# Kernel tuning notes

Hardware: AMD Instinct MI355X
Metric: run time of the kernel (lower is better)

## Reference

```python
import jax, jax.numpy as jnp
import numpy as np

GRID_H, GRID_W, BOX, CLASSES = 13, 13, 5, 80
COORD_FACTOR, NO_OBJECT_FACTOR, OBJECT_FACTOR, CLASS_FACTOR = 1.0, 1.0, 5.0, 1.0
ANCHORS = jnp.array([0.57273, 0.677385, 1.87446, 2.06253, 3.33843, 5.47434,
                     7.88282, 3.52778, 9.77052, 9.16828], dtype=jnp.float32)


def setup_inputs() -> dict:
    key = jax.random.key(0)
    k1, k2, k3 = jax.random.split(key, 3)
    B, T = 256, 50
    y_true = jax.random.uniform(k1, (B, GRID_H, GRID_W, BOX, 5 + CLASSES), dtype=jnp.float32)
    y_pred = jax.random.normal(k2, (B, GRID_H, GRID_W, BOX, 5 + CLASSES), dtype=jnp.float32)
    true_boxes = jax.random.uniform(k3, (B, 1, 1, 1, T, 4), dtype=jnp.float32)
    return {"y_true": y_true, "y_pred": y_pred, "true_boxes": true_boxes}


def reference(y_true, y_pred, true_boxes):
    f32 = jnp.float32
    anchors = ANCHORS.reshape(1, 1, 1, BOX, 2)
    # cell grid exactly as in torch: tile(range(13), 13).reshape(1,13,13,1,1)
    cell_w = jnp.tile(jnp.arange(GRID_H, dtype=f32), (GRID_W,)).reshape(1, GRID_H, GRID_W, 1, 1)
    cell_h = jnp.transpose(cell_w, (0, 2, 1, 3, 4))
    cell_grid = jnp.concatenate([cell_w, cell_h], axis=-1)  # [1,13,13,1,2]

    pred_box_xy = jax.nn.sigmoid(y_pred[..., :2]) + cell_grid          # [B,13,13,5,2]
    pred_box_wh = jnp.exp(y_pred[..., 2:4]) * anchors                  # [B,13,13,5,2]
    pred_box_conf = jax.nn.sigmoid(y_pred[..., 4])                      # [B,13,13,5]
    pred_box_class = y_pred[..., 5:]                                    # [B,13,13,5,80]

    true_box_xy = y_true[..., 0:2]
    true_box_wh = y_true[..., 2:4]

    # IoU between pred and matched true box per anchor cell
    t_half = true_box_wh / 2.0
    t_mins, t_maxes = true_box_xy - t_half, true_box_xy + t_half
    p_half = pred_box_wh / 2.0
    p_mins, p_maxes = pred_box_xy - p_half, pred_box_xy + p_half
    i_wh = jnp.maximum(jnp.minimum(p_maxes, t_maxes) - jnp.maximum(p_mins, t_mins), 0.0)
    i_areas = i_wh[..., 0] * i_wh[..., 1]
    union = pred_box_wh[..., 0] * pred_box_wh[..., 1] + true_box_wh[..., 0] * true_box_wh[..., 1] - i_areas
    iou = i_areas / union
    true_box_conf = iou * y_true[..., 4]
    true_box_class = jnp.argmax(y_true[..., 5:], axis=-1)               # [B,13,13,5]

    coord_mask = y_true[..., 4:5] * COORD_FACTOR                        # [B,13,13,5,1]

    # broadcast IoU vs all true boxes -> [B,13,13,5,T]
    tb_xy, tb_wh = true_boxes[..., 0:2], true_boxes[..., 2:4]
    tb_half = tb_wh / 2.0
    tb_mins, tb_maxes = tb_xy - tb_half, tb_xy + tb_half
    pxy = pred_box_xy[:, :, :, :, None, :]                               # [B,13,13,5,1,2]
    pwh = pred_box_wh[:, :, :, :, None, :]
    pw_half = pwh / 2.0
    pb_mins, pb_maxes = pxy - pw_half, pxy + pw_half
    bi_wh = jnp.maximum(jnp.minimum(pb_maxes, tb_maxes) - jnp.maximum(pb_mins, tb_mins), 0.0)
    bi_areas = bi_wh[..., 1] * bi_wh[..., 0]
    b_union = pwh[..., 0] * pwh[..., 1] + tb_wh[..., 0] * tb_wh[..., 1] - bi_areas
    best_ious = jnp.max(bi_areas / b_union, axis=4)                      # [B,13,13,5]

    conf_mask = (best_ious < 0.6).astype(f32) * (1.0 - y_true[..., 4]) * NO_OBJECT_FACTOR
    conf_mask = conf_mask + true_box_conf * OBJECT_FACTOR
    class_mask = y_true[..., 4] * CLASS_FACTOR

    nb_coord = jnp.sum((coord_mask > 0.0).astype(f32))
    nb_conf = jnp.sum((conf_mask > 0.0).astype(f32))
    nb_class = jnp.sum((class_mask > 0.0).astype(f32))

    loss_xy = jnp.sum(jnp.square(true_box_xy - pred_box_xy) * coord_mask) / (nb_coord + 1e-6) / 2.0
    loss_wh = jnp.sum(jnp.square(true_box_wh - pred_box_wh) * coord_mask) / (nb_coord + 1e-6) / 2.0
    loss_conf = jnp.sum(jnp.square(true_box_conf - pred_box_conf) * conf_mask) / (nb_conf + 1e-6) / 2.0

    logp = jax.nn.log_softmax(pred_box_class, axis=-1)                   # [B,13,13,5,80]
    ce = -jnp.take_along_axis(logp, true_box_class[..., None], axis=-1)[..., 0]
    loss_class = jnp.sum(ce * class_mask) / (nb_class + 1e-6)

    return loss_xy + loss_wh + loss_conf + loss_class
```

## Files before the change

kernel.cpp:

```cpp
#include <hip/hip_runtime.h>
#include <math.h>

#define GRID_HW   13
#define NBOX      5
#define NCLASS    80
#define REC       85
#define CPB_CELLS (GRID_HW*GRID_HW*NBOX)
#define T_BOXES   50
#define CPB       64
#define THREADS   256

__device__ __constant__ float c_anchors[10] = {
    0.57273f, 0.677385f, 1.87446f, 2.06253f, 3.33843f,
    5.47434f, 7.88282f, 3.52778f, 9.77052f, 9.16828f};

template <int USE_ATOMIC>
__global__ __launch_bounds__(THREADS)
void yolo_loss_main(const float* __restrict__ y_true,
                    const float* __restrict__ y_pred,
                    const float* __restrict__ tboxes,
                    double* __restrict__ partials,
                    int n_cells)
{
    __shared__ float lds_yt[CPB * REC];
    __shared__ float lds_yp[CPB * REC];
    __shared__ double red[4][7];

    const int tid   = threadIdx.x;
    const int cell0 = blockIdx.x * CPB;

    {
        const size_t base = (size_t)cell0 * REC;
        long long avail_ll = (long long)n_cells * REC - (long long)base;
        int navail = (avail_ll > (long long)(CPB * REC)) ? (CPB * REC)
                    : (avail_ll < 0 ? 0 : (int)avail_ll);
        int n4 = navail >> 2;
        const float4* gt = (const float4*)(y_true + base);
        const float4* gp = (const float4*)(y_pred + base);
        float4* st = (float4*)lds_yt;
        float4* sp = (float4*)lds_yp;
        for (int i = tid; i < n4; i += THREADS) { st[i] = gt[i]; sp[i] = gp[i]; }
        for (int i = (n4 << 2) + tid; i < navail; i += THREADS) {
            lds_yt[i] = y_true[base + i];
            lds_yp[i] = y_pred[base + i];
        }
    }
    __syncthreads();

    const int q    = tid & 3;
    const int quad = tid >> 2;
    const int cell = cell0 + quad;

    double p_xy = 0.0, p_wh = 0.0, p_conf = 0.0, p_ce = 0.0;
    double p_nc = 0.0, p_nf = 0.0, p_ncl = 0.0;

    if (cell < n_cells) {
        int b    = cell / CPB_CELLS;
        int rem  = cell - b * CPB_CELLS;
        int h    = rem / (GRID_HW * NBOX);
        int rem2 = rem - h * (GRID_HW * NBOX);
        int w    = rem2 / NBOX;
        int box  = rem2 - w * NBOX;

        const float* yt = lds_yt + quad * REC;
        const float* yp = lds_yp + quad * REC;

        const float yt4 = yt[4];
        const float tx = yt[0], ty = yt[1], tw = yt[2], th = yt[3];

        const float px = 1.f / (1.f + expf(-yp[0])) + (float)w;
        const float py = 1.f / (1.f + expf(-yp[1])) + (float)h;
        const float pw = expf(yp[2]) * c_anchors[2 * box];
        const float ph = expf(yp[3]) * c_anchors[2 * box + 1];
        const float pconf = 1.f / (1.f + expf(-yp[4]));

        const float pw2 = pw * 0.5f, ph2 = ph * 0.5f;
        const float p_minx = px - pw2, p_maxx = px + pw2;
        const float p_miny = py - ph2, p_maxy = py + ph2;

        float tw2 = tw * 0.5f, th2 = th * 0.5f;
        float iw = fmaxf(fminf(p_maxx, tx + tw2) - fmaxf(p_minx, tx - tw2), 0.f);
        float ih = fmaxf(fminf(p_maxy, ty + th2) - fmaxf(p_miny, ty - th2), 0.f);
        float inter = iw * ih;
        float iou = inter / (pw * ph + tw * th - inter);
        const float true_conf = iou * yt4;

        float amax = -INFINITY; int aidx = 0x7fffffff;
        #pragma unroll
        for (int k = 0; k < NCLASS / 4; ++k) {
            int c = q + 4 * k;
            float v = yt[5 + c];
            if (v > amax) { amax = v; aidx = c; }
        }
        #pragma unroll
        for (int m = 1; m <= 2; m <<= 1) {
            float ov = __shfl_xor(amax, m);
            int   oi = __shfl_xor(aidx, m);
            if (ov > amax || (ov == amax && oi < aidx)) { amax = ov; aidx = oi; }
        }

        float lmax = -INFINITY;
        #pragma unroll
        for (int k = 0; k < NCLASS / 4; ++k)
            lmax = fmaxf(lmax, yp[5 + q + 4 * k]);
        #pragma unroll
        for (int m = 1; m <= 2; m <<= 1)
            lmax = fmaxf(lmax, __shfl_xor(lmax, m));
        float lsum = 0.f;
        #pragma unroll
        for (int k = 0; k < NCLASS / 4; ++k)
            lsum += expf(yp[5 + q + 4 * k] - lmax);
        #pragma unroll
        for (int m = 1; m <= 2; m <<= 1)
            lsum += __shfl_xor(lsum, m);
        const float ce = -(yp[5 + aidx] - lmax - logf(lsum));

        const float4* tb = (const float4*)(tboxes + (size_t)b * T_BOXES * 4);
        float best = -INFINITY;
        for (int t = q; t < T_BOXES; t += 4) {
            float4 bx = tb[t];
            float bw2 = bx.z * 0.5f, bh2 = bx.w * 0.5f;
            float iw2 = fmaxf(fminf(p_maxx, bx.x + bw2) - fmaxf(p_minx, bx.x - bw2), 0.f);
            float ih2 = fmaxf(fminf(p_maxy, bx.y + bh2) - fmaxf(p_miny, bx.y - bh2), 0.f);
            float ia = iw2 * ih2;
            float r  = ia / (pw * ph + bx.z * bx.w - ia);
            best = fmaxf(best, r);
        }
        #pragma unroll
        for (int m = 1; m <= 2; m <<= 1)
            best = fmaxf(best, __shfl_xor(best, m));

        if (q == 0) {
            const float cm = yt4;
            p_xy = (double)(((tx - px) * (tx - px) + (ty - py) * (ty - py)) * cm);
            p_wh = (double)(((tw - pw) * (tw - pw) + (th - ph) * (th - ph)) * cm);
            float conf_mask = ((best < 0.6f) ? 1.f : 0.f) * (1.f - yt4)
                            + true_conf * 5.f;
            p_conf = (double)((true_conf - pconf) * (true_conf - pconf) * conf_mask);
            p_ce   = (double)(ce * yt4);
            p_nc   = (cm > 0.f)        ? 1.0 : 0.0;
            p_nf   = (conf_mask > 0.f) ? 1.0 : 0.0;
            p_ncl  = (yt4 > 0.f)       ? 1.0 : 0.0;
        }
    }

    double v[7] = {p_xy, p_wh, p_conf, p_ce, p_nc, p_nf, p_ncl};
    #pragma unroll
    for (int k = 0; k < 7; ++k) {
        #pragma unroll
        for (int off = 32; off > 0; off >>= 1)
            v[k] += __shfl_down(v[k], off);
    }
    const int wave = tid >> 6, lane = tid & 63;
    if (lane == 0) {
        #pragma unroll
        for (int k = 0; k < 7; ++k) red[wave][k] = v[k];
    }
    __syncthreads();
    if (tid < 7) {
        double s = red[0][tid] + red[1][tid] + red[2][tid] + red[3][tid];
        if (USE_ATOMIC) {
            unsafeAtomicAdd(&partials[tid], s);
        } else {
            partials[(size_t)blockIdx.x * 8 + tid] = s;
        }
    }
}

template <int USE_ATOMIC>
__global__ __launch_bounds__(256)
void yolo_loss_final(const double* __restrict__ partials,
                     float* __restrict__ out, int nblocks)
{
    __shared__ double red[4][7];
    const int tid = threadIdx.x;
    double v[7] = {0, 0, 0, 0, 0, 0, 0};
    if (USE_ATOMIC) {
        if (tid < 7) v[0] = partials[tid];
        if (tid == 0) {
        }
        if (tid == 0) {
            double nbc  = partials[4] + 1e-6;
            double nbf  = partials[5] + 1e-6;
            double nbcl = partials[6] + 1e-6;
            out[0] = (float)(partials[0] / nbc * 0.5 + partials[1] / nbc * 0.5 +
                             partials[2] / nbf * 0.5 + partials[3] / nbcl);
        }
        return;
    }
    for (int i = tid; i < nblocks; i += 256) {
        const double* p = partials + (size_t)i * 8;
        #pragma unroll
        for (int k = 0; k < 7; ++k) v[k] += p[k];
    }
    #pragma unroll
    for (int k = 0; k < 7; ++k) {
        #pragma unroll
        for (int off = 32; off > 0; off >>= 1)
            v[k] += __shfl_down(v[k], off);
    }
    const int wave = tid >> 6, lane = tid & 63;
    if (lane == 0) {
        #pragma unroll
        for (int k = 0; k < 7; ++k) red[wave][k] = v[k];
    }
    __syncthreads();
    if (tid == 0) {
        double s[7];
        #pragma unroll
        for (int k = 0; k < 7; ++k)
            s[k] = red[0][k] + red[1][k] + red[2][k] + red[3][k];
        double nbc  = s[4] + 1e-6;
        double nbf  = s[5] + 1e-6;
        double nbcl = s[6] + 1e-6;
        out[0] = (float)(s[0] / nbc * 0.5 + s[1] / nbc * 0.5 +
                         s[2] / nbf * 0.5 + s[3] / nbcl);
    }
}

extern "C" void kernel_launch(void* const* d_in, const int* in_sizes, int n_in,
                              void* d_out, int out_size, void* d_ws, size_t ws_size,
                              hipStream_t stream)
{
    const float* y_true = (const float*)d_in[0];
    const float* y_pred = (const float*)d_in[1];
    const float* tboxes = (const float*)d_in[2];
    float* out  = (float*)d_out;
    double* ws  = (double*)d_ws;

    const int n_cells = in_sizes[0] / REC;
    const int blocks  = (n_cells + CPB - 1) / CPB;
    const size_t need = (size_t)blocks * 8 * sizeof(double);

    if (ws_size >= need) {
        yolo_loss_main<0><<<blocks, THREADS, 0, stream>>>(y_true, y_pred, tboxes, ws, n_cells);
        yolo_loss_final<0><<<1, 256, 0, stream>>>(ws, out, blocks);
    } else {
        hipMemsetAsync(d_ws, 0, 7 * sizeof(double), stream);
        yolo_loss_main<1><<<blocks, THREADS, 0, stream>>>(y_true, y_pred, tboxes, ws, n_cells);
        yolo_loss_final<1><<<1, 256, 0, stream>>>(ws, out, blocks);
    }
}
```

Measured before the change: 195.2 us.

## Read cell records directly from global memory instead of staging through LDS

Removes the cooperative LDS staging of y_true/y_pred records and the block barrier, so each quad of threads loads its cell's fields straight from global memory, relying on caches. It also fuses the argmax and logit-max loops, adds an occupancy hint to launch bounds, and widens the final reduction to 1024 threads with double4 loads over zero-padded partial slots. Dropping the staging frees LDS and the sync, but the per-thread strided global loads (stride 85 floats) are uncoalesced and may rely heavily on L1/L2 to avoid repeated traffic.

```diff
diff --git a/kernel.cpp b/kernel.cpp
--- a/kernel.cpp
+++ b/kernel.cpp
@@ -7,49 +7,27 @@
 #define REC       85
 #define CPB_CELLS (GRID_HW*GRID_HW*NBOX)
 #define T_BOXES   50
-#define CPB       64
 #define THREADS   256
+#define QPB       (THREADS/4)
 
 __device__ __constant__ float c_anchors[10] = {
     0.57273f, 0.677385f, 1.87446f, 2.06253f, 3.33843f,
     5.47434f, 7.88282f, 3.52778f, 9.77052f, 9.16828f};
 
 template <int USE_ATOMIC>
-__global__ __launch_bounds__(THREADS)
+__global__ __launch_bounds__(THREADS, 6)
 void yolo_loss_main(const float* __restrict__ y_true,
                     const float* __restrict__ y_pred,
                     const float* __restrict__ tboxes,
                     double* __restrict__ partials,
                     int n_cells)
 {
-    __shared__ float lds_yt[CPB * REC];
-    __shared__ float lds_yp[CPB * REC];
-    __shared__ double red[4][7];
-
-    const int tid   = threadIdx.x;
-    const int cell0 = blockIdx.x * CPB;
-
-    {
-        const size_t base = (size_t)cell0 * REC;
-        long long avail_ll = (long long)n_cells * REC - (long long)base;
-        int navail = (avail_ll > (long long)(CPB * REC)) ? (CPB * REC)
-                    : (avail_ll < 0 ? 0 : (int)avail_ll);
-        int n4 = navail >> 2;
-        const float4* gt = (const float4*)(y_true + base);
-        const float4* gp = (const float4*)(y_pred + base);
-        float4* st = (float4*)lds_yt;
-        float4* sp = (float4*)lds_yp;
-        for (int i = tid; i < n4; i += THREADS) { st[i] = gt[i]; sp[i] = gp[i]; }
-        for (int i = (n4 << 2) + tid; i < navail; i += THREADS) {
-            lds_yt[i] = y_true[base + i];
-            lds_yp[i] = y_pred[base + i];
-        }
-    }
-    __syncthreads();
-
+    __shared__ double red[4][8];
+
+    const int tid  = threadIdx.x;
     const int q    = tid & 3;
     const int quad = tid >> 2;
-    const int cell = cell0 + quad;
+    const int cell = blockIdx.x * QPB + quad;
 
     double p_xy = 0.0, p_wh = 0.0, p_conf = 0.0, p_ce = 0.0;
     double p_nc = 0.0, p_nf = 0.0, p_ncl = 0.0;
@@ -62,17 +40,17 @@
         int w    = rem2 / NBOX;
         int box  = rem2 - w * NBOX;
 
-        const float* yt = lds_yt + quad * REC;
-        const float* yp = lds_yp + quad * REC;
-
-        const float yt4 = yt[4];
-        const float tx = yt[0], ty = yt[1], tw = yt[2], th = yt[3];
-
-        const float px = 1.f / (1.f + expf(-yp[0])) + (float)w;
-        const float py = 1.f / (1.f + expf(-yp[1])) + (float)h;
-        const float pw = expf(yp[2]) * c_anchors[2 * box];
-        const float ph = expf(yp[3]) * c_anchors[2 * box + 1];
-        const float pconf = 1.f / (1.f + expf(-yp[4]));
+        const float* __restrict__ yt = y_true + (size_t)cell * REC;
+        const float* __restrict__ yp = y_pred + (size_t)cell * REC;
+
+        const float tx = yt[0], ty = yt[1], tw = yt[2], th = yt[3], yt4 = yt[4];
+        const float r0 = yp[0], r1 = yp[1], r2 = yp[2], r3 = yp[3], r4 = yp[4];
+
+        const float px = 1.f / (1.f + expf(-r0)) + (float)w;
+        const float py = 1.f / (1.f + expf(-r1)) + (float)h;
+        const float pw = expf(r2) * c_anchors[2 * box];
+        const float ph = expf(r3) * c_anchors[2 * box + 1];
+        const float pconf = 1.f / (1.f + expf(-r4));
 
         const float pw2 = pw * 0.5f, ph2 = ph * 0.5f;
         const float p_minx = px - pw2, p_maxx = px + pw2;
@@ -86,26 +64,23 @@
         const float true_conf = iou * yt4;
 
         float amax = -INFINITY; int aidx = 0x7fffffff;
+        float lmax = -INFINITY;
         #pragma unroll
         for (int k = 0; k < NCLASS / 4; ++k) {
             int c = q + 4 * k;
-            float v = yt[5 + c];
-            if (v > amax) { amax = v; aidx = c; }
+            float tv = yt[5 + c];
+            float pv = yp[5 + c];
+            if (tv > amax) { amax = tv; aidx = c; }
+            lmax = fmaxf(lmax, pv);
         }
         #pragma unroll
         for (int m = 1; m <= 2; m <<= 1) {
             float ov = __shfl_xor(amax, m);
             int   oi = __shfl_xor(aidx, m);
             if (ov > amax || (ov == amax && oi < aidx)) { amax = ov; aidx = oi; }
-        }
-
-        float lmax = -INFINITY;
-        #pragma unroll
-        for (int k = 0; k < NCLASS / 4; ++k)
-            lmax = fmaxf(lmax, yp[5 + q + 4 * k]);
-        #pragma unroll
-        for (int m = 1; m <= 2; m <<= 1)
             lmax = fmaxf(lmax, __shfl_xor(lmax, m));
+        }
+
         float lsum = 0.f;
         #pragma unroll
         for (int k = 0; k < NCLASS / 4; ++k)
@@ -117,6 +92,7 @@
 
         const float4* tb = (const float4*)(tboxes + (size_t)b * T_BOXES * 4);
         float best = -INFINITY;
+        #pragma unroll 2
         for (int t = q; t < T_BOXES; t += 4) {
             float4 bx = tb[t];
             float bw2 = bx.z * 0.5f, bh2 = bx.w * 0.5f;
@@ -157,10 +133,11 @@
         for (int k = 0; k < 7; ++k) red[wave][k] = v[k];
     }
     __syncthreads();
-    if (tid < 7) {
-        double s = red[0][tid] + red[1][tid] + red[2][tid] + red[3][tid];
+    if (tid < 8) {
+        double s = (tid < 7) ? (red[0][tid] + red[1][tid] + red[2][tid] + red[3][tid])
+                             : 0.0;
         if (USE_ATOMIC) {
-            unsafeAtomicAdd(&partials[tid], s);
+            if (tid < 7) unsafeAtomicAdd(&partials[tid], s);
         } else {
             partials[(size_t)blockIdx.x * 8 + tid] = s;
         }
@@ -168,17 +145,14 @@
 }
 
 template <int USE_ATOMIC>
-__global__ __launch_bounds__(256)
+__global__ __launch_bounds__(1024)
 void yolo_loss_final(const double* __restrict__ partials,
                      float* __restrict__ out, int nblocks)
 {
-    __shared__ double red[4][7];
+    __shared__ double red[16][8];
     const int tid = threadIdx.x;
-    double v[7] = {0, 0, 0, 0, 0, 0, 0};
+
     if (USE_ATOMIC) {
-        if (tid < 7) v[0] = partials[tid];
-        if (tid == 0) {
-        }
         if (tid == 0) {
             double nbc  = partials[4] + 1e-6;
             double nbf  = partials[5] + 1e-6;
@@ -188,10 +162,14 @@
         }
         return;
     }
-    for (int i = tid; i < nblocks; i += 256) {
-        const double* p = partials + (size_t)i * 8;
-        #pragma unroll
-        for (int k = 0; k < 7; ++k) v[k] += p[k];
+
+    double v[7] = {0, 0, 0, 0, 0, 0, 0};
+    for (int i = tid; i < nblocks; i += 1024) {
+        const double4* p = (const double4*)(partials + (size_t)i * 8);
+        double4 a = p[0];
+        double4 b = p[1];
+        v[0] += a.x; v[1] += a.y; v[2] += a.z; v[3] += a.w;
+        v[4] += b.x; v[5] += b.y; v[6] += b.z;
     }
     #pragma unroll
     for (int k = 0; k < 7; ++k) {
@@ -208,8 +186,12 @@
     if (tid == 0) {
         double s[7];
         #pragma unroll
-        for (int k = 0; k < 7; ++k)
-            s[k] = red[0][k] + red[1][k] + red[2][k] + red[3][k];
+        for (int k = 0; k < 7; ++k) {
+            double acc = 0.0;
+            #pragma unroll
+            for (int wv = 0; wv < 16; ++wv) acc += red[wv][k];
+            s[k] = acc;
+        }
         double nbc  = s[4] + 1e-6;
         double nbf  = s[5] + 1e-6;
         double nbcl = s[6] + 1e-6;
@@ -229,15 +211,15 @@
     double* ws  = (double*)d_ws;
 
     const int n_cells = in_sizes[0] / REC;
-    const int blocks  = (n_cells + CPB - 1) / CPB;
+    const int blocks  = (n_cells + QPB - 1) / QPB;
     const size_t need = (size_t)blocks * 8 * sizeof(double);
 
     if (ws_size >= need) {
         yolo_loss_main<0><<<blocks, THREADS, 0, stream>>>(y_true, y_pred, tboxes, ws, n_cells);
-        yolo_loss_final<0><<<1, 256, 0, stream>>>(ws, out, blocks);
+        yolo_loss_final<0><<<1, 1024, 0, stream>>>(ws, out, blocks);
     } else {
         hipMemsetAsync(d_ws, 0, 7 * sizeof(double), stream);
         yolo_loss_main<1><<<blocks, THREADS, 0, stream>>>(y_true, y_pred, tboxes, ws, n_cells);
-        yolo_loss_final<1><<<1, 256, 0, stream>>>(ws, out, blocks);
+        yolo_loss_final<1><<<1, 64, 0, stream>>>(ws, out, blocks);
     }
 }
```

Result: faster. 183.4 us (-6.0%).
